# Optimization experiments

Hardware: AMD Instinct MI355X
Metric: run time of the kernel (lower is better)

## Reference

```python
import jax, jax.numpy as jnp
import numpy as np

ALPHA = 0.2  # LeakyReLU negative slope from init kwarg
NEG_INF = -9e15


def gat_multihead(x, adj_mask, W, a, concat):
    """Standard (GLMP-style) dense GAT, all heads at once.
    x: [B,N,Din], adj_mask: [B,N,N] bool, W: [H,Din,F], a: [H,2F].
    """
    B, N, _ = x.shape
    H, _, F = W.shape
    Wh = jnp.einsum('bnd,hdf->bhnf', x, W)              # [B,H,N,F]
    f1 = jnp.einsum('bhnf,hf->bhn', Wh, a[:, :F])
    f2 = jnp.einsum('bhnf,hf->bhn', Wh, a[:, F:])
    e = jax.nn.leaky_relu(f1[:, :, :, None] + f2[:, :, None, :], ALPHA)  # [B,H,N,N]
    e = jnp.where(adj_mask[:, None], e, NEG_INF)
    att = jax.nn.softmax(e, axis=-1)
    out = jnp.einsum('bhij,bhjf->bhif', att, Wh)        # [B,H,N,F]
    if concat:
        out = jax.nn.elu(out)
        return out.transpose(0, 2, 1, 3).reshape(B, N, H * F)
    # concat=False heads are summed and divided by nheads in load_graph -> mean
    return out.mean(axis=1)


def setup_inputs() -> dict:
    key = jax.random.key(0)
    ks = jax.random.split(key, 12)
    B, N, T = 16, 1024, 6
    V, D, F, H = 32000, 128, 64, 4
    CONV_MAX = 400
    story = jax.random.randint(ks[0], (B, N, T), 0, V)
    kb_len = jax.random.randint(ks[1], (B,), 1, CONV_MAX)
    conv_len = jax.random.randint(ks[2], (B,), 1, CONV_MAX)
    hidden = jax.random.normal(ks[3], (B, F), dtype=jnp.float32)
    dh_outputs = jax.random.normal(ks[4], (B, CONV_MAX, D), dtype=jnp.float32)
    adj = (jax.random.uniform(ks[5], (B, N, N)) < 0.05).astype(jnp.float32)
    emb = jax.random.normal(ks[6], (V, D), dtype=jnp.float32) * 0.1
    W1 = jax.random.normal(ks[7], (H, D, F), dtype=jnp.float32) * 0.1
    a1 = jax.random.normal(ks[8], (H, 2 * F), dtype=jnp.float32) * 0.1
    W2 = jax.random.normal(ks[9], (H, H * F, F), dtype=jnp.float32) * 0.1
    a2 = jax.random.normal(ks[10], (H, 2 * F), dtype=jnp.float32) * 0.1
    W3 = jax.random.normal(ks[11], (H, H * F, F), dtype=jnp.float32) * 0.1
    a3 = jax.random.normal(jax.random.fold_in(key, 99), (H, 2 * F), dtype=jnp.float32) * 0.1
    return {"story": story, "kb_len": kb_len, "conv_len": conv_len,
            "hidden": hidden, "dh_outputs": dh_outputs, "adj": adj,
            "emb": emb, "W1": W1, "a1": a1, "W2": W2, "a2": a2, "W3": W3, "a3": a3}


def reference(story, kb_len, conv_len, hidden, dh_outputs, adj, emb, W1, a1, W2, a2, W3, a3):
    B, N, T = story.shape
    Lc = dh_outputs.shape[1]
    # Embedding lookup + bag-of-words sum over memory token slots
    x = emb[story].sum(axis=2)                              # [B,N,D]
    # add_lm_embedding: scatter dh_outputs[b, :conv_len[b]] into slots
    # [kb_len[b]-1, kb_len[b]-1+conv_len[b]) of the memory (vectorized)
    pos = jnp.arange(N)[None, :]                            # [1,N]
    off = pos - (kb_len[:, None] - 1)                       # [B,N]
    valid = (off >= 0) & (off < conv_len[:, None])
    idx = jnp.clip(off, 0, Lc - 1)
    gathered = jnp.take_along_axis(dh_outputs, idx[:, :, None], axis=1)  # [B,N,D]
    x = x + jnp.where(valid[:, :, None], gathered, 0.0)
    # update_pad_token_adj: self-loop for pad slots k >= kb_len+conv_len
    d = jnp.arange(N)
    start = kb_len + conv_len                               # (kb_len-1)+conv_len+1
    diag = adj[:, d, d]
    adj = adj.at[:, d, d].set(jnp.where(d[None, :] >= start[:, None], 1.0, diag))
    adj_mask = adj > 0
    # Three GAT stacks (dropout omitted: eval mode)
    x = gat_multihead(x, adj_mask, W1, a1, concat=True)     # [B,N,H*F]
    x = gat_multihead(x, adj_mask, W2, a2, concat=True)     # [B,N,H*F]
    x = jax.nn.sigmoid(gat_multihead(x, adj_mask, W3, a3, concat=False))  # [B,N,F]
    prob_logits = jnp.einsum('bnf,bf->bn', x, hidden)       # [B,N]
    return (jax.nn.sigmoid(prob_logits), hidden, prob_logits)
```

## Files before the change

### kernel.cpp

```cpp
#include <hip/hip_runtime.h>
#include <stdint.h>

typedef short bf16x8 __attribute__((ext_vector_type(8)));
typedef float f32x4 __attribute__((ext_vector_type(4)));
typedef unsigned short u16;
typedef unsigned short u16x4 __attribute__((ext_vector_type(4)));
typedef unsigned int u32;
typedef unsigned int u32x4 __attribute__((ext_vector_type(4)));
typedef unsigned long long u64;


__device__ inline u16 f2b(float f) {
    unsigned u = __float_as_uint(f);
    u += 0x7fffu + ((u >> 16) & 1u);
    return (u16)(u >> 16);
}

__device__ inline float wred_sum(float v) {
    #pragma unroll
    for (int m = 32; m >= 1; m >>= 1) v += __shfl_xor(v, m, 64);
    return v;
}

__global__ __launch_bounds__(256) void k_pre(const float* __restrict__ adj,
                                             const int* __restrict__ kb,
                                             const int* __restrict__ cv,
                                             const int* __restrict__ story,
                                             const float* __restrict__ dh,
                                             const float* __restrict__ emb,
                                             const float* __restrict__ W1,
                                             const float* __restrict__ a1,
                                             const float* __restrict__ W2,
                                             const float* __restrict__ a2,
                                             const float* __restrict__ W3,
                                             const float* __restrict__ a3,
                                             u64* __restrict__ mask,
                                             u16* __restrict__ x0,
                                             u16* __restrict__ Bp1,
                                             u16* __restrict__ Bp2,
                                             u16* __restrict__ Bp3,
                                             float* __restrict__ d0g) {
    int bid = blockIdx.x;
    int tid = threadIdx.x;
    if (bid < 2048) {
        int w = tid >> 6, l = tid & 63;
        int rbase = (bid << 3) + (w << 1);
        int b = rbase >> 10;
        int start = kb[b] + cv[b];
        const float4* a4 = (const float4*)adj;
        u16* mask16 = (u16*)mask;
        #pragma unroll
        for (int r = 0; r < 2; ++r) {
            int row = rbase + r;
            int i = row & 1023;
            size_t base = (size_t)row * 256 + (l << 2);
            float4 v0 = a4[base + 0];
            float4 v1 = a4[base + 1];
            float4 v2 = a4[base + 2];
            float4 v3 = a4[base + 3];
            u32 m16 = 0;
            m16 |= (u32)(v0.x > 0.0f) << 0;  m16 |= (u32)(v0.y > 0.0f) << 1;
            m16 |= (u32)(v0.z > 0.0f) << 2;  m16 |= (u32)(v0.w > 0.0f) << 3;
            m16 |= (u32)(v1.x > 0.0f) << 4;  m16 |= (u32)(v1.y > 0.0f) << 5;
            m16 |= (u32)(v1.z > 0.0f) << 6;  m16 |= (u32)(v1.w > 0.0f) << 7;
            m16 |= (u32)(v2.x > 0.0f) << 8;  m16 |= (u32)(v2.y > 0.0f) << 9;
            m16 |= (u32)(v2.z > 0.0f) << 10; m16 |= (u32)(v2.w > 0.0f) << 11;
            m16 |= (u32)(v3.x > 0.0f) << 12; m16 |= (u32)(v3.y > 0.0f) << 13;
            m16 |= (u32)(v3.z > 0.0f) << 14; m16 |= (u32)(v3.w > 0.0f) << 15;
            if (i >= start && (i >> 4) == l) m16 |= 1u << (i & 15);
            u64 bal = __ballot(m16 != 0);
            mask16[(size_t)row * 64 + l] = (u16)m16;
            if (l == 0) d0g[row] = (bal == 0ull) ? 1.0f : 0.0f;
        }
    } else if (bid < 4096) {
        int w = tid >> 6, l = tid & 63;
        int r = l >> 5, dq = l & 31;
        int bn = ((bid - 2048) << 3) + (w << 1) + r;
        int b = bn >> 10, n = bn & 1023;
        const int2* st2 = (const int2*)(story + (size_t)bn * 6);
        int2 s01 = st2[0], s23 = st2[1], s45 = st2[2];
        int toks[6] = {s01.x, s01.y, s23.x, s23.y, s45.x, s45.y};
        const float4* emb4 = (const float4*)emb;
        float4 acc = {0.f, 0.f, 0.f, 0.f};
        #pragma unroll
        for (int t = 0; t < 6; ++t) {
            float4 e = emb4[(size_t)toks[t] * 32 + dq];
            acc.x += e.x; acc.y += e.y; acc.z += e.z; acc.w += e.w;
        }
        int off = n - (kb[b] - 1);
        if (off >= 0 && off < cv[b]) {
            float4 d = ((const float4*)dh)[((size_t)b * 400 + off) * 32 + dq];
            acc.x += d.x; acc.y += d.y; acc.z += d.z; acc.w += d.w;
        }
        u16x4 pk = {f2b(acc.x), f2b(acc.y), f2b(acc.z), f2b(acc.w)};
        *(u16x4*)(x0 + ((size_t)bn << 7) + (dq << 2)) = pk;
    } else {
        int pb = bid - 4096;
        const float *W, *a; u16* Bp; int K;
        if (pb < 136)      { W = W1; a = a1; Bp = Bp1; K = 128; }
        else if (pb < 408) { W = W2; a = a2; Bp = Bp2; K = 256; pb -= 136; }
        else               { W = W3; a = a3; Bp = Bp3; K = 256; pb -= 408; }
        int id = pb * 256 + tid;
        int j = id & 7, lane = (id >> 3) & 63, fr = id >> 9;
        int kt = fr / 17, ct = fr - kt * 17;
        int kk = (kt << 5) + ((lane >> 4) << 3) + j;
        u16 o;
        if (ct < 16) {
            int col = (ct << 4) | (lane & 15);
            o = f2b(W[((size_t)(col >> 6) * K + kk) * 64 + (col & 63)]);
        } else {
            int c = lane & 15;
            if (c < 8) {
                int h = c >> 1, wh = c & 1;
                const float4* wr = (const float4*)(W + ((size_t)h * K + kk) * 64);
                const float4* av = (const float4*)(a + h * 128 + wh * 64);
                float s = 0.0f;
                #pragma unroll
                for (int q = 0; q < 16; ++q) {
                    float4 x = wr[q], y = av[q];
                    s += x.x * y.x + x.y * y.y + x.z * y.z + x.w * y.w;
                }
                o = f2b(s);
            } else o = 0;
        }
        Bp[id] = o;
    }
}

template <int KT>
__global__ __launch_bounds__(256) void k_gemm(const u16* __restrict__ A,
                                              const u16* __restrict__ Bp,
                                              u16* __restrict__ WhB,
                                              float* __restrict__ f1,
                                              float* __restrict__ f2) {
    constexpr int K = KT * 32;
    __shared__ __align__(16) u16 tile[4][2][2048];
    int tid = threadIdx.x, w = tid >> 6, l = tid & 63;
    int rtp = blockIdx.x;
    int colq = w;
    int m0 = rtp << 5;
    int b = m0 >> 10, n0 = m0 & 1023;
    int jt = n0 >> 5;
    const bf16x8* Av = (const bf16x8*)A;
    const bf16x8* Bv = (const bf16x8*)Bp;
    int arowA = m0 + (l & 15);
    bf16x8 afA[KT], afB[KT];
    #pragma unroll
    for (int kt = 0; kt < KT; ++kt) {
        size_t base = ((size_t)arowA * K + (kt << 5) + ((l >> 4) << 3)) >> 3;
        afA[kt] = Av[base];
        afB[kt] = Av[base + ((16 * K) >> 3)];
    }
    f32x4 accA[4], accB[4];
    #pragma unroll
    for (int c = 0; c < 4; ++c) { accA[c] = f32x4{0.f,0.f,0.f,0.f}; accB[c] = f32x4{0.f,0.f,0.f,0.f}; }
    f32x4 acc16A = {0.f,0.f,0.f,0.f}, acc16B = {0.f,0.f,0.f,0.f};
    #pragma unroll
    for (int kt = 0; kt < KT; ++kt) {
        #pragma unroll
        for (int c = 0; c < 4; ++c) {
            bf16x8 bv = Bv[(size_t)(kt * 17 + (colq << 2) + c) * 64 + l];
            accA[c] = __builtin_amdgcn_mfma_f32_16x16x32_bf16(afA[kt], bv, accA[c], 0, 0, 0);
            accB[c] = __builtin_amdgcn_mfma_f32_16x16x32_bf16(afB[kt], bv, accB[c], 0, 0, 0);
        }
        if (colq == 0) {
            bf16x8 bv = Bv[(size_t)(kt * 17 + 16) * 64 + l];
            acc16A = __builtin_amdgcn_mfma_f32_16x16x32_bf16(afA[kt], bv, acc16A, 0, 0, 0);
            acc16B = __builtin_amdgcn_mfma_f32_16x16x32_bf16(afB[kt], bv, acc16B, 0, 0, 0);
        }
    }
    int co = l & 15, ro = (l >> 4) << 2;
    if (colq == 0 && co < 8) {
        int hh = co >> 1;
        float* fp = (co & 1) ? f2 : f1;
        int base = (((b << 2) + hh) << 10) + n0 + ro;
        #pragma unroll
        for (int r = 0; r < 4; ++r) {
            fp[base + r] = acc16A[r];
            fp[base + 16 + r] = acc16B[r];
        }
    }
    u16* twA = tile[w][0]; u16* twB = tile[w][1];
    #pragma unroll
    for (int c = 0; c < 4; ++c) {
        int col2 = (c << 4) + co;
        u16x4 pkA, pkB;
        #pragma unroll
        for (int r = 0; r < 4; ++r) { pkA[r] = f2b(accA[c][r]); pkB[r] = f2b(accB[c][r]); }
        *(u16x4*)(twA + (col2 << 4) + ro) = pkA;
        *(u16x4*)(twB + (col2 << 4) + ro) = pkB;
    }
    __syncthreads();
    int bh = (b << 2) + colq;
    int lq = l & 31;
    #pragma unroll
    for (int ftq = 0; ftq < 2; ++ftq) {
        int ft = (ftq << 1) + (l >> 5);
        int col2 = (ft << 4) + (l & 15);
        int r0 = ((l >> 4) & 1) << 3;
        bf16x8 vA = *(const bf16x8*)(twA + (col2 << 4) + r0);
        bf16x8 vB = *(const bf16x8*)(twB + (col2 << 4) + r0);
        size_t fidx = (size_t)((bh << 7) + (jt << 2) + ft);
        *(bf16x8*)(WhB + (fidx * 64 + lq) * 8) = vA;
        *(bf16x8*)(WhB + (fidx * 64 + 32 + lq) * 8) = vB;
    }
}

#define PV_HALF(f2v4, m4, jh, f1i, d0f, fragbase, Bv, acc, accs, g, row)         \
    {                                                                            \
        u32 onep = ((row) == 0) ? 0x3F803F80u : 0u;                              \
        u32x4 ov = {onep, onep, onep, onep};                                     \
        bf16x8 sfrag = __builtin_bit_cast(bf16x8, ov);                           \
        u32x4 mwq;                                                               \
        for (int t = 0; t < 16; ++t) {                                           \
            if ((t & 3) == 0) mwq = (m4)[t >> 2];                                \
            int jtg = ((jh) << 4) + t;                                           \
            u32 sh = mwq[t & 3] >> ((g) << 3);                                   \
            f32x4 fa = (f2v4)[(jtg << 3) + ((g) << 1)];                          \
            f32x4 fb = (f2v4)[(jtg << 3) + ((g) << 1) + 1];                      \
            float p[8];                                                          \
            _Pragma("unroll")                                                    \
            for (int jj = 0; jj < 8; ++jj) {                                     \
                float f2j = (jj < 4) ? fa[jj] : fb[jj - 4];                      \
                float tt = (f1i) + f2j;                                          \
                float e = fmaxf(tt, 0.2f * tt);                                  \
                float ex;                                                        \
                asm("v_exp_f32 %0, %1" : "=v"(ex) : "v"(e));                     \
                p[jj] = (sh & (1u << jj)) ? ex : (d0f);                          \
            }                                                                    \
            u32x4 pk;                                                            \
            _Pragma("unroll")                                                    \
            for (int q = 0; q < 4; ++q) {                                        \
                u32 r;                                                           \
                asm("v_cvt_pk_bf16_f32 %0, %1, %2"                               \
                    : "=v"(r) : "v"(p[2 * q]), "v"(p[2 * q + 1]));               \
                pk[q] = r;                                                       \
            }                                                                    \
            bf16x8 af = __builtin_bit_cast(bf16x8, pk);                          \
            accs = __builtin_amdgcn_mfma_f32_16x16x32_bf16(af, sfrag, accs, 0, 0, 0); \
            _Pragma("unroll")                                                    \
            for (int ft = 0; ft < 4; ++ft)                                       \
                acc[ft] = __builtin_amdgcn_mfma_f32_16x16x32_bf16(               \
                    af, Bv[(size_t)((fragbase) + (jtg << 2) + ft) * 64 + l], acc[ft], 0, 0, 0); \
        }                                                                        \
    }

__global__ __launch_bounds__(256, 8) void k_pv0(const u32* __restrict__ mask32,
                                                const float* __restrict__ f1g,
                                                const float* __restrict__ f2g,
                                                const float* __restrict__ d0g,
                                                const bf16x8* __restrict__ Bv,
                                                u16* __restrict__ xout) {
    __shared__ __align__(16) float f2s[1024];
    __shared__ float comb[2][20][64];
    const float LOG2E = 1.44269504088896340736f;
    int tid = threadIdx.x;
    int w = tid >> 6, l = tid & 63;
    int bh = blockIdx.x >> 5;
    int b = bh >> 2, h = bh & 3;
    int slot = w >> 1, jh = w & 1;
    int itile = ((blockIdx.x & 31) << 1) + slot;
    int i0 = itile << 4;
    for (int idx = tid; idx < 1024; idx += 256) f2s[idx] = f2g[(bh << 10) + idx] * LOG2E;
    __syncthreads();
    int row = l & 15, g = l >> 4;
    int i = i0 + row;
    float f1i = f1g[(bh << 10) + i] * LOG2E;
    float d0f = d0g[(b << 10) + i];
    const u32x4* m4 = (const u32x4*)(mask32 + (((size_t)(b << 10) + i) << 5)) + (jh << 2);
    f32x4 acc[4];
    #pragma unroll
    for (int ft = 0; ft < 4; ++ft) acc[ft] = f32x4{0.f, 0.f, 0.f, 0.f};
    f32x4 accs = {0.f, 0.f, 0.f, 0.f};
    const f32x4* f2v4 = (const f32x4*)f2s;
    int fragbase = bh << 7;
    PV_HALF(f2v4, m4, jh, f1i, d0f, fragbase, Bv, acc, accs, g, row)
    if (jh == 1) {
        #pragma unroll
        for (int v = 0; v < 16; ++v) comb[slot][v][l] = acc[v >> 2][v & 3];
        #pragma unroll
        for (int r = 0; r < 4; ++r) comb[slot][16 + r][l] = accs[r];
    }
    __syncthreads();
    if (jh == 0) {
        #pragma unroll
        for (int v = 0; v < 16; ++v) acc[v >> 2][v & 3] += comb[slot][v][l];
        #pragma unroll
        for (int r = 0; r < 4; ++r) accs[r] += comb[slot][16 + r][l];
        #pragma unroll
        for (int reg = 0; reg < 4; ++reg) {
            int orow = (g << 2) + reg;
            float s = __shfl(accs[reg], g << 4, 64);
            float rinv = 1.0f / s;
            int grow = i0 + orow;
            #pragma unroll
            for (int ft = 0; ft < 4; ++ft) {
                float v = acc[ft][reg] * rinv;
                float e2 = v > 0.0f ? v : (__expf(v) - 1.0f);
                xout[((size_t)((b << 10) + grow) << 8) + (h << 6) + (ft << 4) + row] = f2b(e2);
            }
        }
    }
}

__global__ __launch_bounds__(512, 8) void k_pv3(const u32* __restrict__ mask32,
                                                const float* __restrict__ f1g,
                                                const float* __restrict__ f2g,
                                                const float* __restrict__ d0g,
                                                const bf16x8* __restrict__ Bv,
                                                const float* __restrict__ hidden,
                                                float* __restrict__ dout) {
    __shared__ __align__(16) float shbuf[4096];
    __shared__ float comb[4][20][64];
    const float LOG2E = 1.44269504088896340736f;
    int tid = threadIdx.x;
    int w = tid >> 6, l = tid & 63;
    int b = blockIdx.x >> 6;
    int itile = blockIdx.x & 63;
    int i0 = itile << 4;
    int h = w >> 1, jh = w & 1;
    int bh = (b << 2) + h;
    for (int idx = tid; idx < 4096; idx += 512) shbuf[idx] = f2g[(b << 12) + idx] * LOG2E;
    __syncthreads();
    int row = l & 15, g = l >> 4;
    int i = i0 + row;
    float f1i = f1g[(bh << 10) + i] * LOG2E;
    float d0f = d0g[(b << 10) + i];
    const u32x4* m4 = (const u32x4*)(mask32 + (((size_t)(b << 10) + i) << 5)) + (jh << 2);
    f32x4 acc[4];
    #pragma unroll
    for (int ft = 0; ft < 4; ++ft) acc[ft] = f32x4{0.f, 0.f, 0.f, 0.f};
    f32x4 accs = {0.f, 0.f, 0.f, 0.f};
    const f32x4* f2v4 = (const f32x4*)(shbuf + (h << 10));
    int fragbase = bh << 7;
    PV_HALF(f2v4, m4, jh, f1i, d0f, fragbase, Bv, acc, accs, g, row)
    if (jh == 1) {
        #pragma unroll
        for (int v = 0; v < 16; ++v) comb[h][v][l] = acc[v >> 2][v & 3];
        #pragma unroll
        for (int r = 0; r < 4; ++r) comb[h][16 + r][l] = accs[r];
    }
    __syncthreads();
    if (jh == 0) {
        #pragma unroll
        for (int v = 0; v < 16; ++v) acc[v >> 2][v & 3] += comb[h][v][l];
        #pragma unroll
        for (int r = 0; r < 4; ++r) accs[r] += comb[h][16 + r][l];
        #pragma unroll
        for (int reg = 0; reg < 4; ++reg) {
            int orow = (g << 2) + reg;
            float s = __shfl(accs[reg], g << 4, 64);
            float rinv = 1.0f / s;
            #pragma unroll
            for (int ft = 0; ft < 4; ++ft)
                shbuf[(h << 10) + (orow << 6) + (ft << 4) + row] = acc[ft][reg] * rinv;
        }
    }
    __syncthreads();
    float hid = hidden[(b << 6) + l];
    #pragma unroll
    for (int k = 0; k < 2; ++k) {
        int rl = (k << 3) + w;
        int o = (rl << 6) + l;
        float s = shbuf[o] + shbuf[1024 + o] + shbuf[2048 + o] + shbuf[3072 + o];
        s *= 0.25f;
        float x = 1.0f / (1.0f + __expf(-s));
        float logit = wred_sum(x * hid);
        if (l == 0) {
            int grow = i0 + rl;
            dout[(b << 10) + grow] = 1.0f / (1.0f + __expf(-logit));
            dout[17408 + (b << 10) + grow] = logit;
        }
    }
    if (itile == 0 && w == 0) dout[16384 + (b << 6) + l] = hid;
}

extern "C" void kernel_launch(void* const* d_in, const int* in_sizes, int n_in,
                              void* d_out, int out_size, void* d_ws, size_t ws_size,
                              hipStream_t stream) {
    const int*   story  = (const int*)d_in[0];
    const int*   kb     = (const int*)d_in[1];
    const int*   cv     = (const int*)d_in[2];
    const float* hidden = (const float*)d_in[3];
    const float* dh     = (const float*)d_in[4];
    const float* adj    = (const float*)d_in[5];
    const float* emb    = (const float*)d_in[6];
    const float* W1     = (const float*)d_in[7];
    const float* a1     = (const float*)d_in[8];
    const float* W2     = (const float*)d_in[9];
    const float* a2     = (const float*)d_in[10];
    const float* W3     = (const float*)d_in[11];
    const float* a3     = (const float*)d_in[12];
    float* dout = (float*)d_out;

    char* ws = (char*)d_ws;
    u64*   mask   = (u64*)(ws + 0);
    u32*   mask32 = (u32*)(ws + 0);
    u16*   x0   = (u16*)(ws + 2097152);
    u16*   xbf  = (u16*)(ws + 6291456);
    u16*   WhB  = (u16*)(ws + 14680064);
    float* f1   = (float*)(ws + 23068672);
    float* f2   = (float*)(ws + 23330816);
    u16*   Bp1  = (u16*)(ws + 23592960);
    u16*   Bp2  = (u16*)(ws + 23662592);
    u16*   Bp3  = (u16*)(ws + 23801856);
    float* d0g  = (float*)(ws + 23941120);

    k_pre<<<4776, 256, 0, stream>>>(adj, kb, cv, story, dh, emb,
                                    W1, a1, W2, a2, W3, a3,
                                    mask, x0, Bp1, Bp2, Bp3, d0g);

    k_gemm<4><<<512, 256, 0, stream>>>(x0, Bp1, WhB, f1, f2);
    k_pv0<<<2048, 256, 0, stream>>>(mask32, f1, f2, d0g, (const bf16x8*)WhB, xbf);

    k_gemm<8><<<512, 256, 0, stream>>>(xbf, Bp2, WhB, f1, f2);
    k_pv0<<<2048, 256, 0, stream>>>(mask32, f1, f2, d0g, (const bf16x8*)WhB, xbf);

    k_gemm<8><<<512, 256, 0, stream>>>(xbf, Bp3, WhB, f1, f2);
    k_pv3<<<1024, 512, 0, stream>>>(mask32, f1, f2, d0g, (const bf16x8*)WhB, hidden, dout);
}
```

Baseline: 144.2 us.

## Factor LeakyReLU-softmax exponent into precomputed per-row and per-column exponentials

```diff
diff --git a/kernel.cpp b/kernel.cpp
--- a/kernel.cpp
+++ b/kernel.cpp
@@ -20,6 +20,20 @@
     #pragma unroll
     for (int m = 32; m >= 1; m >>= 1) v += __shfl_xor(v, m, 64);
     return v;
+}
+
+__device__ inline float exp2_fast(float x) {
+    float r;
+    asm("v_exp_f32 %0, %1" : "=v"(r) : "v"(x));
+    return r;
+}
+
+__device__ inline u32 packexp(float v) {
+    const float LOG2E  = 1.44269504088896340736f;
+    const float LOG2E5 = 0.28853900817779268147f;
+    u16 lo = f2b(exp2_fast(v * LOG2E));
+    u16 hi = f2b(exp2_fast(v * LOG2E5));
+    return (u32)lo | ((u32)hi << 16);
 }
 
 __global__ __launch_bounds__(256) void k_pre(const float* __restrict__ adj,
@@ -206,7 +220,7 @@
     }
 }
 
-#define PV_HALF(f2v4, m4, jh, f1i, d0f, fragbase, Bv, acc, accs, g, row)         \
+#define PV_HALF(f2c4, m4, jh, e1p, e1q, d0f, fragbase, Bv, acc, accs, g, row)    \
     {                                                                            \
         u32 onep = ((row) == 0) ? 0x3F803F80u : 0u;                              \
         u32x4 ov = {onep, onep, onep, onep};                                     \
@@ -216,17 +230,16 @@
             if ((t & 3) == 0) mwq = (m4)[t >> 2];                                \
             int jtg = ((jh) << 4) + t;                                           \
             u32 sh = mwq[t & 3] >> ((g) << 3);                                   \
-            f32x4 fa = (f2v4)[(jtg << 3) + ((g) << 1)];                          \
-            f32x4 fb = (f2v4)[(jtg << 3) + ((g) << 1) + 1];                      \
+            u32x4 ca = (f2c4)[(jtg << 3) + ((g) << 1)];                          \
+            u32x4 cb = (f2c4)[(jtg << 3) + ((g) << 1) + 1];                      \
             float p[8];                                                          \
             _Pragma("unroll")                                                    \
             for (int jj = 0; jj < 8; ++jj) {                                     \
-                float f2j = (jj < 4) ? fa[jj] : fb[jj - 4];                      \
-                float tt = (f1i) + f2j;                                          \
-                float e = fmaxf(tt, 0.2f * tt);                                  \
-                float ex;                                                        \
-                asm("v_exp_f32 %0, %1" : "=v"(ex) : "v"(e));                     \
-                p[jj] = (sh & (1u << jj)) ? ex : (d0f);                          \
+                u32 c = (jj < 4) ? ca[jj] : cb[jj - 4];                          \
+                float ep = __uint_as_float(c << 16);                             \
+                float eq = __uint_as_float(c & 0xFFFF0000u);                     \
+                float v = fmaxf((e1p) * ep, (e1q) * eq);                         \
+                p[jj] = (sh & (1u << jj)) ? v : (d0f);                           \
             }                                                                    \
             u32x4 pk;                                                            \
             _Pragma("unroll")                                                    \
@@ -251,9 +264,10 @@
                                                 const float* __restrict__ d0g,
                                                 const bf16x8* __restrict__ Bv,
                                                 u16* __restrict__ xout) {
-    __shared__ __align__(16) float f2s[1024];
+    __shared__ __align__(16) u32 f2c[1024];
     __shared__ float comb[2][20][64];
-    const float LOG2E = 1.44269504088896340736f;
+    const float LOG2E  = 1.44269504088896340736f;
+    const float LOG2E5 = 0.28853900817779268147f;
     int tid = threadIdx.x;
     int w = tid >> 6, l = tid & 63;
     int bh = blockIdx.x >> 5;
@@ -261,20 +275,22 @@
     int slot = w >> 1, jh = w & 1;
     int itile = ((blockIdx.x & 31) << 1) + slot;
     int i0 = itile << 4;
-    for (int idx = tid; idx < 1024; idx += 256) f2s[idx] = f2g[(bh << 10) + idx] * LOG2E;
+    for (int idx = tid; idx < 1024; idx += 256) f2c[idx] = packexp(f2g[(bh << 10) + idx]);
     __syncthreads();
     int row = l & 15, g = l >> 4;
     int i = i0 + row;
-    float f1i = f1g[(bh << 10) + i] * LOG2E;
+    float f1i = f1g[(bh << 10) + i];
+    float e1p = exp2_fast(f1i * LOG2E);
+    float e1q = exp2_fast(f1i * LOG2E5);
     float d0f = d0g[(b << 10) + i];
     const u32x4* m4 = (const u32x4*)(mask32 + (((size_t)(b << 10) + i) << 5)) + (jh << 2);
     f32x4 acc[4];
     #pragma unroll
     for (int ft = 0; ft < 4; ++ft) acc[ft] = f32x4{0.f, 0.f, 0.f, 0.f};
     f32x4 accs = {0.f, 0.f, 0.f, 0.f};
-    const f32x4* f2v4 = (const f32x4*)f2s;
+    const u32x4* f2c4 = (const u32x4*)f2c;
     int fragbase = bh << 7;
-    PV_HALF(f2v4, m4, jh, f1i, d0f, fragbase, Bv, acc, accs, g, row)
+    PV_HALF(f2c4, m4, jh, e1p, e1q, d0f, fragbase, Bv, acc, accs, g, row)
     if (jh == 1) {
         #pragma unroll
         for (int v = 0; v < 16; ++v) comb[slot][v][l] = acc[v >> 2][v & 3];
@@ -310,9 +326,10 @@
                                                 const bf16x8* __restrict__ Bv,
                                                 const float* __restrict__ hidden,
                                                 float* __restrict__ dout) {
-    __shared__ __align__(16) float shbuf[4096];
+    __shared__ __align__(16) u32 shbuf[4096];
     __shared__ float comb[4][20][64];
-    const float LOG2E = 1.44269504088896340736f;
+    const float LOG2E  = 1.44269504088896340736f;
+    const float LOG2E5 = 0.28853900817779268147f;
     int tid = threadIdx.x;
     int w = tid >> 6, l = tid & 63;
     int b = blockIdx.x >> 6;
@@ -320,20 +337,22 @@
     int i0 = itile << 4;
     int h = w >> 1, jh = w & 1;
     int bh = (b << 2) + h;
-    for (int idx = tid; idx < 4096; idx += 512) shbuf[idx] = f2g[(b << 12) + idx] * LOG2E;
+    for (int idx = tid; idx < 4096; idx += 512) shbuf[idx] = packexp(f2g[(b << 12) + idx]);
     __syncthreads();
     int row = l & 15, g = l >> 4;
     int i = i0 + row;
-    float f1i = f1g[(bh << 10) + i] * LOG2E;
+    float f1i = f1g[(bh << 10) + i];
+    float e1p = exp2_fast(f1i * LOG2E);
+    float e1q = exp2_fast(f1i * LOG2E5);
     float d0f = d0g[(b << 10) + i];
     const u32x4* m4 = (const u32x4*)(mask32 + (((size_t)(b << 10) + i) << 5)) + (jh << 2);
     f32x4 acc[4];
     #pragma unroll
     for (int ft = 0; ft < 4; ++ft) acc[ft] = f32x4{0.f, 0.f, 0.f, 0.f};
     f32x4 accs = {0.f, 0.f, 0.f, 0.f};
-    const f32x4* f2v4 = (const f32x4*)(shbuf + (h << 10));
+    const u32x4* f2c4 = (const u32x4*)(shbuf + (h << 10));
     int fragbase = bh << 7;
-    PV_HALF(f2v4, m4, jh, f1i, d0f, fragbase, Bv, acc, accs, g, row)
+    PV_HALF(f2c4, m4, jh, e1p, e1q, d0f, fragbase, Bv, acc, accs, g, row)
     if (jh == 1) {
         #pragma unroll
         for (int v = 0; v < 16; ++v) comb[h][v][l] = acc[v >> 2][v & 3];
@@ -341,6 +360,7 @@
         for (int r = 0; r < 4; ++r) comb[h][16 + r][l] = accs[r];
     }
     __syncthreads();
+    float* outb = (float*)shbuf;
     if (jh == 0) {
         #pragma unroll
         for (int v = 0; v < 16; ++v) acc[v >> 2][v & 3] += comb[h][v][l];
@@ -353,7 +373,7 @@
             float rinv = 1.0f / s;
             #pragma unroll
             for (int ft = 0; ft < 4; ++ft)
-                shbuf[(h << 10) + (orow << 6) + (ft << 4) + row] = acc[ft][reg] * rinv;
+                outb[(h << 10) + (orow << 6) + (ft << 4) + row] = acc[ft][reg] * rinv;
         }
     }
     __syncthreads();
@@ -362,7 +382,7 @@
     for (int k = 0; k < 2; ++k) {
         int rl = (k << 3) + w;
         int o = (rl << 6) + l;
-        float s = shbuf[o] + shbuf[1024 + o] + shbuf[2048 + o] + shbuf[3072 + o];
+        float s = outb[o] + outb[1024 + o] + outb[2048 + o] + outb[3072 + o];
         s *= 0.25f;
         float x = 1.0f / (1.0f + __expf(-s));
         float logit = wred_sum(x * hid);
```

Measured after the change: 144.2 us. No clear change (+0.0%).
